# Kernel tuning notes

Measured on AMD Instinct MI355X. Metric: run time of the kernel, lower is better.

The kernel has to match this reference:

```python
import jax, jax.numpy as jnp
import numpy as np

NHEAD = 6
EPS = 1.1920929e-07  # torch RMSNorm default eps = finfo(float32).eps


def _rms(x, g):
    return x * jax.lax.rsqrt(jnp.mean(x * x, axis=-1, keepdims=True) + EPS) * g


def _mha(q, k, v):
    # q: [B, Sq, Hq, D]; k, v: [B, Sk, Hk, D] with Hk == Hq or Hk == 1 (broadcast)
    d = q.shape[-1]
    qh = q.transpose(0, 2, 1, 3)            # [B, Hq, Sq, D]
    kh = k.transpose(0, 2, 1, 3)            # [B, Hk, Sk, D]
    vh = v.transpose(0, 2, 1, 3)
    s = jnp.matmul(qh, kh.transpose(0, 1, 3, 2)) * (1.0 / np.sqrt(d).astype(np.float32))
    a = jax.nn.softmax(s, axis=-1)
    return jnp.matmul(a, vh).transpose(0, 2, 1, 3)  # [B, Sq, Hq, D]


def setup_inputs() -> dict:
    key = jax.random.key(0)
    B, R, G, E, L = 4, 1024, 8, 192, 4
    F = 2 * E  # dim_feedforward = emsize * 2
    ks = jax.random.split(key, 12)

    def w(k, shape):
        return jax.random.normal(k, shape, jnp.float32) * 0.02

    return {
        "hidden": jax.random.normal(ks[0], (B, R, G, E), jnp.float32),
        "Wq1": w(ks[1], (L, E, E)), "Wk1": w(ks[2], (L, E, E)),
        "Wv1": w(ks[3], (L, E, E)), "Wo1": w(ks[4], (L, E, E)),
        "Wq2": w(ks[5], (L, E, E)), "Wk2": w(ks[6], (L, E, E)),
        "Wv2": w(ks[7], (L, E, E)), "Wo2": w(ks[8], (L, E, E)),
        "W1": w(ks[9], (L, E, F)), "W2": w(ks[10], (L, F, E)),
        "g1": jnp.ones((L, E), jnp.float32),
        "g2": jnp.ones((L, E), jnp.float32),
        "g3": jnp.ones((L, E), jnp.float32),
        "single_eval_pos": 768,
    }


def reference(hidden, Wq1, Wk1, Wv1, Wo1, Wq2, Wk2, Wv2, Wo2, W1, W2, g1, g2, g3, single_eval_pos):
    B, R, G, E = hidden.shape
    H, D = NHEAD, E // NHEAD
    sep = int(single_eval_pos)
    L = Wq1.shape[0]
    x = hidden
    for i in range(L):
        # --- per-sample attention between feature groups: seqs of length G ---
        xf = x.reshape(B * R, G, E)
        q = (xf @ Wq1[i]).reshape(B * R, G, H, D)
        k = (xf @ Wk1[i]).reshape(B * R, G, H, D)
        v = (xf @ Wv1[i]).reshape(B * R, G, H, D)
        xf = xf + _mha(q, k, v).reshape(B * R, G, E) @ Wo1[i]
        # --- along-column attention over rows with train/test split ---
        xr = _rms(xf, g1[i]).reshape(B, R, G, E).transpose(0, 2, 1, 3).reshape(B * G, R, E)
        q = (xr @ Wq2[i]).reshape(B * G, R, H, D)
        k = (xr[:, :sep] @ Wk2[i]).reshape(B * G, sep, H, D)
        v = (xr[:, :sep] @ Wv2[i]).reshape(B * G, sep, H, D)
        train_out = _mha(q[:, :sep], k, v)
        # test rows attend to first head's keys/values only (broadcast over heads)
        test_out = _mha(q[:, sep:], k[:, :, :1], v[:, :, :1])
        attn = jnp.concatenate([train_out, test_out], axis=1).reshape(B * G, R, E) @ Wo2[i]
        xc = _rms(xr + attn, g2[i])
        # --- MLP (exact GELU) + final RMSNorm ---
        x = xc.reshape(B, G, R, E).transpose(0, 2, 1, 3)
        x = x + jax.nn.gelu(x @ W1[i], approximate=False) @ W2[i]
        x = _rms(x, g3[i])
    return x
```

## Files before the change

### kernel.cpp

```cpp
#include <hip/hip_runtime.h>
#include <hip/hip_bf16.h>
#include <math.h>

#define B_ 4
#define R_ 1024
#define G_ 8
#define E_ 192
#define H_ 6
#define D_ 32
#define L_ 4
#define F_ 384
#define M_ (B_*R_*G_)
static const size_t NBUF = (size_t)M_ * E_;
static const size_t WPL  = 8 * (size_t)E_ * E_ + 2 * (size_t)E_ * F_;

typedef __attribute__((ext_vector_type(8))) short bf16x8;
typedef __attribute__((ext_vector_type(8))) unsigned short u16x8;
typedef __attribute__((ext_vector_type(4))) float f32x4;

__device__ __forceinline__ float gelu_exact(float x) {
    return 0.5f * x * (1.0f + erff(x * 0.7071067811865475f));
}
__device__ __forceinline__ unsigned short f2bf(float f) {
    __hip_bfloat16 h = __float2bfloat16(f);
    return *(unsigned short*)&h;
}
__device__ __forceinline__ float bf2f(unsigned short h) {
    union { unsigned u; float f; } v; v.u = ((unsigned)h) << 16; return v.f;
}
__device__ __forceinline__ bf16x8 mk8(unsigned long long lo, unsigned long long hi) {
    union { unsigned long long q[2]; bf16x8 v; } u;
    u.q[0] = lo; u.q[1] = hi; return u.v;
}

__global__ __launch_bounds__(256)
void k_convw_all(const float* __restrict__ Wq1, const float* __restrict__ Wk1,
                 const float* __restrict__ Wv1, const float* __restrict__ Wo1,
                 const float* __restrict__ Wq2, const float* __restrict__ Wk2,
                 const float* __restrict__ Wv2, const float* __restrict__ Wo2,
                 const float* __restrict__ W1,  const float* __restrict__ W2,
                 unsigned short* __restrict__ Wt)
{
    const int t = blockIdx.x;
    const int layer = t / 432;
    const int r = t % 432;
    const float* src; unsigned short* dst; int K, N; float scale = 1.f; int tile;
    if (r < 288) {
        const int w = r / 36; tile = r % 36; K = E_; N = E_;
        const float* tab[8] = {Wq1, Wk1, Wv1, Wo1, Wq2, Wk2, Wv2, Wo2};
        src = tab[w] + (size_t)layer * E_ * E_;
        dst = Wt + (size_t)layer * WPL + (size_t)w * E_ * E_;
        if (w == 0) scale = 0.17677669529663687f;
        if (w == 4) scale = 0.17677669529663687f * 1.4426950408889634f;
    } else if (r < 360) {
        tile = r - 288; K = E_; N = F_;
        src = W1 + (size_t)layer * E_ * F_;
        dst = Wt + (size_t)layer * WPL + 8 * (size_t)E_ * E_;
    } else {
        tile = r - 360; K = F_; N = E_;
        src = W2 + (size_t)layer * E_ * F_;
        dst = Wt + (size_t)layer * WPL + 8 * (size_t)E_ * E_ + (size_t)E_ * F_;
    }
    const int ntx = N / 32;
    const int kb = (tile / ntx) * 32, nb = (tile % ntx) * 32;
    __shared__ float tl[32][33];
    const int tx = threadIdx.x & 31, ty = threadIdx.x >> 5;
    for (int i2 = 0; i2 < 32; i2 += 8)
        tl[ty + i2][tx] = src[(size_t)(kb + ty + i2) * N + nb + tx];
    __syncthreads();
    for (int i2 = 0; i2 < 32; i2 += 8)
        dst[(size_t)(nb + ty + i2) * K + kb + tx] = f2bf(tl[tx][ty + i2] * scale);
}

template<bool ABF16, int EPI>
__global__ __launch_bounds__(256)
void k_gemm_mfma(const void* __restrict__ Ap, const unsigned short* __restrict__ Wt,
                 void* __restrict__ Cp, int ldc, int K)
{
    __shared__ unsigned short As[64][40];
    __shared__ unsigned short Bs[192][40];
    const int m0 = blockIdx.x * 64;
    const int n0 = blockIdx.y * 192;
    const int tid = threadIdx.x;
    const int w = tid >> 6, lane = tid & 63, l15 = lane & 15, g = lane >> 4;
    const int arow = tid >> 2, akoff = (tid & 3) << 3;
    f32x4 acc[4][3];
#pragma unroll
    for (int mt = 0; mt < 4; ++mt)
#pragma unroll
        for (int nt = 0; nt < 3; ++nt)
#pragma unroll
            for (int r2 = 0; r2 < 4; ++r2) acc[mt][nt][r2] = 0.f;
    const int nK = K >> 5;

    float4 ax, ay; u16x8 av; u16x8 bv0, bv1, bv2;
    auto gload = [&](int k0) {
        if (ABF16) {
            av = *(const u16x8*)((const unsigned short*)Ap + (size_t)(m0 + arow) * K + k0 + akoff);
        } else {
            const float* ap = (const float*)Ap + (size_t)(m0 + arow) * K + k0 + akoff;
            ax = *(const float4*)ap; ay = *(const float4*)(ap + 4);
        }
        bv0 = *(const u16x8*)(Wt + (size_t)(n0 + arow      ) * K + k0 + akoff);
        bv1 = *(const u16x8*)(Wt + (size_t)(n0 + arow +  64) * K + k0 + akoff);
        bv2 = *(const u16x8*)(Wt + (size_t)(n0 + arow + 128) * K + k0 + akoff);
    };
    auto swrite = [&]() {
        u16x8 aw;
        if (ABF16) aw = av;
        else {
            aw[0] = f2bf(ax.x); aw[1] = f2bf(ax.y); aw[2] = f2bf(ax.z); aw[3] = f2bf(ax.w);
            aw[4] = f2bf(ay.x); aw[5] = f2bf(ay.y); aw[6] = f2bf(ay.z); aw[7] = f2bf(ay.w);
        }
        *(u16x8*)&As[arow][akoff] = aw;
        *(u16x8*)&Bs[arow][akoff] = bv0;
        *(u16x8*)&Bs[arow + 64][akoff] = bv1;
        *(u16x8*)&Bs[arow + 128][akoff] = bv2;
    };

    gload(0);
    for (int kc = 0; kc < nK; ++kc) {
        __syncthreads();
        swrite();
        __syncthreads();
        if (kc + 1 < nK) gload((kc + 1) << 5);
        bf16x8 af[4], bfr[3];
#pragma unroll
        for (int mt = 0; mt < 4; ++mt) af[mt] = *(const bf16x8*)&As[mt * 16 + l15][g * 8];
#pragma unroll
        for (int nt = 0; nt < 3; ++nt) bfr[nt] = *(const bf16x8*)&Bs[w * 48 + nt * 16 + l15][g * 8];
#pragma unroll
        for (int mt = 0; mt < 4; ++mt)
#pragma unroll
            for (int nt = 0; nt < 3; ++nt)
                acc[mt][nt] = __builtin_amdgcn_mfma_f32_16x16x32_bf16(af[mt], bfr[nt], acc[mt][nt], 0, 0, 0);
    }

#pragma unroll
    for (int mt = 0; mt < 4; ++mt)
#pragma unroll
        for (int r2 = 0; r2 < 4; ++r2) {
            const int m = m0 + mt * 16 + g * 4 + r2;
#pragma unroll
            for (int nt = 0; nt < 3; ++nt) {
                const int n = w * 48 + nt * 16 + l15;
                float v = acc[mt][nt][r2];
                if (EPI == 1) v = gelu_exact(v);
                ((unsigned short*)Cp)[(size_t)m * ldc + n0 + n] = f2bf(v);
            }
        }
}

template<bool RESBF16, int EPI>
__global__ __launch_bounds__(256)
void k_gemm_rms32(const unsigned short* __restrict__ Ap, const unsigned short* __restrict__ Wt,
                  const void* __restrict__ Resp, const float* __restrict__ gvec,
                  void* __restrict__ Cp, int K)
{
    __shared__ unsigned short As[32][40];
    __shared__ unsigned short Bs[192][40];
    __shared__ float ss_red[4][16];
    const int m0 = blockIdx.x * 32;
    const int tid = threadIdx.x;
    const int w = tid >> 6, lane = tid & 63, l15 = lane & 15, g = lane >> 4;
    const int mt = w & 1, nh = w >> 1;
    const int arow = tid >> 2, akoff = (tid & 3) << 3;
    f32x4 acc[6];
#pragma unroll
    for (int nt = 0; nt < 6; ++nt)
#pragma unroll
        for (int r2 = 0; r2 < 4; ++r2) acc[nt][r2] = 0.f;
    const int nK = K >> 5;

    u16x8 av, bv0, bv1, bv2;
    auto gload = [&](int k0) {
        if (tid < 128)
            av = *(const u16x8*)(Ap + (size_t)(m0 + arow) * K + k0 + akoff);
        bv0 = *(const u16x8*)(Wt + (size_t)(arow      ) * K + k0 + akoff);
        bv1 = *(const u16x8*)(Wt + (size_t)(arow +  64) * K + k0 + akoff);
        bv2 = *(const u16x8*)(Wt + (size_t)(arow + 128) * K + k0 + akoff);
    };
    auto swrite = [&]() {
        if (tid < 128) *(u16x8*)&As[arow][akoff] = av;
        *(u16x8*)&Bs[arow][akoff] = bv0;
        *(u16x8*)&Bs[arow + 64][akoff] = bv1;
        *(u16x8*)&Bs[arow + 128][akoff] = bv2;
    };

    gload(0);
    for (int kc = 0; kc < nK; ++kc) {
        __syncthreads();
        swrite();
        __syncthreads();
        if (kc + 1 < nK) gload((kc + 1) << 5);
        bf16x8 af = *(const bf16x8*)&As[mt * 16 + l15][g * 8];
        bf16x8 bfr[6];
#pragma unroll
        for (int nt = 0; nt < 6; ++nt) bfr[nt] = *(const bf16x8*)&Bs[nh * 96 + nt * 16 + l15][g * 8];
#pragma unroll
        for (int nt = 0; nt < 6; ++nt)
            acc[nt] = __builtin_amdgcn_mfma_f32_16x16x32_bf16(af, bfr[nt], acc[nt], 0, 0, 0);
    }

    float ssp[4] = {0.f, 0.f, 0.f, 0.f};
#pragma unroll
    for (int r2 = 0; r2 < 4; ++r2) {
        const int m = m0 + mt * 16 + g * 4 + r2;
#pragma unroll
        for (int nt = 0; nt < 6; ++nt) {
            const int n = nh * 96 + nt * 16 + l15;
            float rres = RESBF16 ? bf2f(((const unsigned short*)Resp)[(size_t)m * E_ + n])
                                 : ((const float*)Resp)[(size_t)m * E_ + n];
            float v = acc[nt][r2] + rres;
            acc[nt][r2] = v;
            ssp[r2] += v * v;
        }
    }
#pragma unroll
    for (int off = 1; off < 16; off <<= 1)
#pragma unroll
        for (int r2 = 0; r2 < 4; ++r2)
            ssp[r2] += __shfl_xor(ssp[r2], off);
    if (l15 == 0) {
#pragma unroll
        for (int r2 = 0; r2 < 4; ++r2)
            ss_red[w][g * 4 + r2] = ssp[r2];
    }
    __syncthreads();
#pragma unroll
    for (int r2 = 0; r2 < 4; ++r2) {
        const int lr = g * 4 + r2;
        const float ss = ss_red[mt][lr] + ss_red[2 + mt][lr];
        const float inv = rsqrtf(ss * (1.0f / 192.0f) + 1.1920929e-07f);
        const int m = m0 + mt * 16 + lr;
        size_t orow;
        if (EPI == 2) {
            const int b = m >> 13, rr = (m >> 3) & 1023, gg = m & 7;
            orow = (((size_t)b * G_ + gg) << 10) + rr;
        } else if (EPI == 3) {
            const int b = m >> 13, gg = (m >> 10) & 7, rr = m & 1023;
            orow = ((((size_t)b << 10) + rr) << 3) + gg;
        } else {
            orow = m;
        }
#pragma unroll
        for (int nt = 0; nt < 6; ++nt) {
            const int n = nh * 96 + nt * 16 + l15;
            const float v = acc[nt][r2] * inv * gvec[n];
            if (EPI == 4) ((float*)Cp)[orow * E_ + n] = v;
            else          ((unsigned short*)Cp)[orow * E_ + n] = f2bf(v);
        }
    }
}

__global__ __launch_bounds__(256)
void k_attn1(const unsigned short* __restrict__ QKV, unsigned short* __restrict__ T)
{
    const int wave = blockIdx.x * 4 + (threadIdx.x >> 6);
    const int lane = threadIdx.x & 63;
    const int seq = wave / H_;
    const int h = wave % H_;
    const int i = lane >> 3, j = lane & 7;
    const unsigned short* qp = QKV + ((size_t)(seq * G_ + i)) * 576 + h * D_;
    const unsigned short* kp = QKV + ((size_t)(seq * G_ + j)) * 576 + 192 + h * D_;
    float s = 0.f;
#pragma unroll
    for (int d8 = 0; d8 < 4; ++d8) {
        u16x8 qv = *(const u16x8*)(qp + d8 * 8);
        u16x8 kv = *(const u16x8*)(kp + d8 * 8);
#pragma unroll
        for (int e = 0; e < 8; ++e) s += bf2f(qv[e]) * bf2f(kv[e]);
    }
    float mx = s;
#pragma unroll
    for (int off = 1; off < 8; off <<= 1) mx = fmaxf(mx, __shfl_xor(mx, off));
    float p = __expf(s - mx);
    float sum = p;
#pragma unroll
    for (int off = 1; off < 8; off <<= 1) sum += __shfl_xor(sum, off);
    p /= sum;
    const int base = lane & ~7;
    float o0 = 0.f, o1 = 0.f, o2 = 0.f, o3 = 0.f;
#pragma unroll
    for (int jj = 0; jj < 8; ++jj) {
        float pj = __shfl(p, base + jj);
        ushort4 vv = *(const ushort4*)(QKV + ((size_t)(seq * G_ + jj)) * 576 + 384 + h * D_ + j * 4);
        o0 += pj * bf2f(vv.x); o1 += pj * bf2f(vv.y);
        o2 += pj * bf2f(vv.z); o3 += pj * bf2f(vv.w);
    }
    ushort4 ov; ov.x = f2bf(o0); ov.y = f2bf(o1); ov.z = f2bf(o2); ov.w = f2bf(o3);
    *(ushort4*)(T + ((size_t)(seq * G_ + i)) * E_ + h * D_ + j * 4) = ov;
}

__global__ __launch_bounds__(256)
void k_attn2(const unsigned short* __restrict__ QKV, unsigned short* __restrict__ T,
             const int* __restrict__ sep_ptr)
{
    __shared__ __align__(16) unsigned short K_lds[64][40];
    __shared__ __align__(16) unsigned short V_lds[2048];

    const int sep = *sep_ptr;
    const int bid = blockIdx.x;
    const int sh = ((bid >> 7) << 3) | (bid & 7);
    const int qtile = (bid >> 3) & 15;
    const int s = sh / H_, h = sh % H_;
    const int q0 = qtile * 64;

    const int tid = threadIdx.x;
    const int w = tid >> 6;
    const int lane = tid & 63;
    const int l15 = lane & 15;
    const int g = lane >> 4;

    const int qrow = q0 + w * 16 + l15;
    u16x8 qf = *(const u16x8*)(QKV + ((size_t)s * R_ + qrow) * 576 + h * D_ + g * 8);

    u16x8 onesu;
#pragma unroll
    for (int e = 0; e < 8; ++e) onesu[e] = 0x3F80;
    const bf16x8 onesf = (bf16x8)onesu;

    const bool lo = (q0 < sep);
    const bool hi = (q0 + 64 > sep);
    const int npass = (lo && hi) ? 2 : 1;
    const int nChunk = (sep + 63) >> 6;

    const int skey = tid >> 2;
    const int sg   = tid & 3;
    const int vst = ((sg >> 1) * 16 + (skey >> 2)) * 64 + (skey & 3) * 16 + (sg & 1) * 8;
    const unsigned vaddr = (unsigned)(size_t)&V_lds[0] + (unsigned)(g * 128 + l15 * 2);

    for (int pass = 0; pass < npass; ++pass) {
        const int hk = (pass == 0) ? (lo ? h : 0) : 0;
        const unsigned short* Kb = QKV + (size_t)s * R_ * 576 + 192 + hk * D_;
        const unsigned short* Vb = QKV + (size_t)s * R_ * 576 + 384 + hk * D_;

        float mrun = -1e30f;
        f32x4 o0 = {0.f, 0.f, 0.f, 0.f};
        f32x4 o1 = {0.f, 0.f, 0.f, 0.f};
        f32x4 o2 = {0.f, 0.f, 0.f, 0.f};

        u16x8 kv_k = *(const u16x8*)(Kb + (size_t)skey * 576 + sg * 8);
        u16x8 kv_v = *(const u16x8*)(Vb + (size_t)skey * 576 + sg * 8);

        for (int kc = 0; kc < nChunk; ++kc) {
            const int kbase = kc * 64;
            const bool full = (kbase + 64 <= sep);
            __syncthreads();
            *(u16x8*)&K_lds[skey][sg * 8] = kv_k;
            *(u16x8*)&V_lds[vst] = kv_v;
            __syncthreads();
            if (kc + 1 < nChunk) {
                kv_k = *(const u16x8*)(Kb + (size_t)(kbase + 64 + skey) * 576 + sg * 8);
                kv_v = *(const u16x8*)(Vb + (size_t)(kbase + 64 + skey) * 576 + sg * 8);
            }

            f32x4 sc[4];
            const f32x4 zf = {0.f, 0.f, 0.f, 0.f};
            __builtin_amdgcn_s_setprio(1);
#pragma unroll
            for (int t = 0; t < 4; ++t) {
                bf16x8 a = *(const bf16x8*)&K_lds[t * 16 + l15][g * 8];
                sc[t] = __builtin_amdgcn_mfma_f32_16x16x32_bf16(a, (bf16x8)qf, zf, 0, 0, 0);
            }
            __builtin_amdgcn_s_setprio(0);
            if (!full) {
#pragma unroll
                for (int t = 0; t < 4; ++t)
#pragma unroll
                    for (int r = 0; r < 4; ++r)
                        if (kbase + t * 16 + g * 4 + r >= sep) sc[t][r] = -1e30f;
            }
            float mx = fmaxf(fmaxf(sc[0][0], sc[0][1]), sc[0][2]);
            mx = fmaxf(fmaxf(sc[0][3], sc[1][0]), mx);
            mx = fmaxf(fmaxf(sc[1][1], sc[1][2]), mx);
            mx = fmaxf(fmaxf(sc[1][3], sc[2][0]), mx);
            mx = fmaxf(fmaxf(sc[2][1], sc[2][2]), mx);
            mx = fmaxf(fmaxf(sc[2][3], sc[3][0]), mx);
            mx = fmaxf(fmaxf(sc[3][1], sc[3][2]), mx);
            mx = fmaxf(mx, sc[3][3]);
            if (!__all((int)(mx <= mrun + 11.0f))) {
                mx = fmaxf(mx, __shfl_xor(mx, 16));
                mx = fmaxf(mx, __shfl_xor(mx, 32));
                const float mnew = fmaxf(mrun, mx);
                const float scl = exp2f(mrun - mnew);
#pragma unroll
                for (int r = 0; r < 4; ++r) { o0[r] *= scl; o1[r] *= scl; o2[r] *= scl; }
                mrun = mnew;
            }
            bf16x8 pb0, pb1;
            {
                u16x8 p0, p1;
#pragma unroll
                for (int r = 0; r < 4; ++r) {
                    p0[r]     = f2bf(exp2f(sc[0][r] - mrun));
                    p0[4 + r] = f2bf(exp2f(sc[1][r] - mrun));
                    p1[r]     = f2bf(exp2f(sc[2][r] - mrun));
                    p1[4 + r] = f2bf(exp2f(sc[3][r] - mrun));
                }
                pb0 = (bf16x8)p0; pb1 = (bf16x8)p1;
            }
            unsigned long long t0, t1, t2, t3, t4, t5, t6, t7;
            asm volatile(
                "ds_read_b64_tr_b16 %0, %8 offset:0\n\t"
                "ds_read_b64_tr_b16 %1, %8 offset:512\n\t"
                "ds_read_b64_tr_b16 %2, %8 offset:1024\n\t"
                "ds_read_b64_tr_b16 %3, %8 offset:1536\n\t"
                "ds_read_b64_tr_b16 %4, %8 offset:2048\n\t"
                "ds_read_b64_tr_b16 %5, %8 offset:2560\n\t"
                "ds_read_b64_tr_b16 %6, %8 offset:3072\n\t"
                "ds_read_b64_tr_b16 %7, %8 offset:3584\n\t"
                "s_waitcnt lgkmcnt(0)"
                : "=&v"(t0), "=&v"(t1), "=&v"(t2), "=&v"(t3),
                  "=&v"(t4), "=&v"(t5), "=&v"(t6), "=&v"(t7)
                : "v"(vaddr)
                : "memory");
            __builtin_amdgcn_sched_barrier(0);
            __builtin_amdgcn_s_setprio(1);
            o0 = __builtin_amdgcn_mfma_f32_16x16x32_bf16(mk8(t0, t1), pb0, o0, 0, 0, 0);
            o1 = __builtin_amdgcn_mfma_f32_16x16x32_bf16(mk8(t4, t5), pb0, o1, 0, 0, 0);
            o2 = __builtin_amdgcn_mfma_f32_16x16x32_bf16(onesf,       pb0, o2, 0, 0, 0);
            o0 = __builtin_amdgcn_mfma_f32_16x16x32_bf16(mk8(t2, t3), pb1, o0, 0, 0, 0);
            o1 = __builtin_amdgcn_mfma_f32_16x16x32_bf16(mk8(t6, t7), pb1, o1, 0, 0, 0);
            o2 = __builtin_amdgcn_mfma_f32_16x16x32_bf16(onesf,       pb1, o2, 0, 0, 0);
            __builtin_amdgcn_s_setprio(0);
        }

        const bool valid = (npass == 1) || (pass == 0 ? (qrow < sep) : (qrow >= sep));
        if (valid) {
            const float inv = 1.f / o2[0];
            unsigned short* tp = T + ((size_t)s * R_ + qrow) * E_ + h * D_;
            ushort4 v0, v1;
            v0.x = f2bf(o0[0] * inv); v0.y = f2bf(o0[1] * inv);
            v0.z = f2bf(o0[2] * inv); v0.w = f2bf(o0[3] * inv);
            v1.x = f2bf(o1[0] * inv); v1.y = f2bf(o1[1] * inv);
            v1.z = f2bf(o1[2] * inv); v1.w = f2bf(o1[3] * inv);
            *(ushort4*)(tp + g * 4)      = v0;
            *(ushort4*)(tp + 16 + g * 4) = v1;
        }
    }
}

extern "C" void kernel_launch(void* const* d_in, const int* in_sizes, int n_in,
                              void* d_out, int out_size, void* d_ws, size_t ws_size,
                              hipStream_t stream) {
    const float* hidden = (const float*)d_in[0];
    const float* Wq1 = (const float*)d_in[1];
    const float* Wk1 = (const float*)d_in[2];
    const float* Wv1 = (const float*)d_in[3];
    const float* Wo1 = (const float*)d_in[4];
    const float* Wq2 = (const float*)d_in[5];
    const float* Wk2 = (const float*)d_in[6];
    const float* Wv2 = (const float*)d_in[7];
    const float* Wo2 = (const float*)d_in[8];
    const float* W1  = (const float*)d_in[9];
    const float* W2  = (const float*)d_in[10];
    const float* g1  = (const float*)d_in[11];
    const float* g2  = (const float*)d_in[12];
    const float* g3  = (const float*)d_in[13];
    const int*   sep = (const int*)d_in[14];

    float* Xout = (float*)d_out;
    unsigned short* ws = (unsigned short*)d_ws;
    unsigned short* QKVb = ws;
    unsigned short* Tb   = QKVb + (size_t)M_ * 576;
    unsigned short* Ynb  = Tb + NBUF;
    unsigned short* Xcb  = Ynb + NBUF;
    unsigned short* Xb   = Xcb + NBUF;
    unsigned short* Wt   = Xb + NBUF;
    unsigned short* H1b  = QKVb;

    const dim3 blk(256);
    const dim3 gQKV(M_ / 64, 3);
    const dim3 gW1(M_ / 64, 2);
    const dim3 g32(M_ / 32);
    const dim3 gA1((4096 * H_) / 4);
    const dim3 gA2(32 * H_ * 16);

    k_convw_all<<<dim3(432 * L_), blk, 0, stream>>>(Wq1, Wk1, Wv1, Wo1, Wq2, Wk2, Wv2, Wo2, W1, W2, Wt);

    for (int i = 0; i < L_; ++i) {
        unsigned short* wl = Wt + (size_t)i * WPL;
        const unsigned short* wqkv1 = wl;
        const unsigned short* wo1   = wl + 3 * (size_t)E_ * E_;
        const unsigned short* wqkv2 = wl + 4 * (size_t)E_ * E_;
        const unsigned short* wo2   = wl + 7 * (size_t)E_ * E_;
        const unsigned short* w1    = wl + 8 * (size_t)E_ * E_;
        const unsigned short* w2    = wl + 8 * (size_t)E_ * E_ + (size_t)E_ * F_;
        const float* g1i = g1 + (size_t)i * E_;
        const float* g2i = g2 + (size_t)i * E_;
        const float* g3i = g3 + (size_t)i * E_;

        if (i == 0)
            k_gemm_mfma<false, 0><<<gQKV, blk, 0, stream>>>(hidden, wqkv1, QKVb, 576, E_);
        else
            k_gemm_mfma<true, 0><<<gQKV, blk, 0, stream>>>(Xb, wqkv1, QKVb, 576, E_);
        k_attn1<<<gA1, blk, 0, stream>>>(QKVb, Tb);
        if (i == 0)
            k_gemm_rms32<false, 2><<<g32, blk, 0, stream>>>(Tb, wo1, hidden, g1i, Ynb, E_);
        else
            k_gemm_rms32<true, 2><<<g32, blk, 0, stream>>>(Tb, wo1, Xb, g1i, Ynb, E_);
        k_gemm_mfma<true, 0><<<gQKV, blk, 0, stream>>>(Ynb, wqkv2, QKVb, 576, E_);
        k_attn2<<<gA2, blk, 0, stream>>>(QKVb, Tb, sep);
        k_gemm_rms32<true, 3><<<g32, blk, 0, stream>>>(Tb, wo2, Ynb, g2i, Xcb, E_);
        k_gemm_mfma<true, 1><<<gW1, blk, 0, stream>>>(Xcb, w1, H1b, F_, E_);
        if (i == L_ - 1)
            k_gemm_rms32<true, 4><<<g32, blk, 0, stream>>>(H1b, w2, Xcb, g3i, Xout, F_);
        else
            k_gemm_rms32<true, 5><<<g32, blk, 0, stream>>>(H1b, w2, Xcb, g3i, Xb, F_);
    }
}
```

Measured before the change: 683.1 us.

## Process two query tiles per wave in column attention to reuse K/V LDS loads

Each attention block now covers 128 query rows instead of 64, with every wave handling two 16-row query fragments against the same K and V fragments read from LDS. The aim is to halve global K/V loads and LDS staging per query row and to amortise the sync and LDS reads across more MFMA work. In exchange, register pressure rises from the doubled accumulators and the grid is halved, which lowers parallelism and occupancy. The NBUF change is cosmetic.

```diff
diff --git a/kernel.cpp b/kernel.cpp
--- a/kernel.cpp
+++ b/kernel.cpp
@@ -11,7 +11,7 @@
 #define L_ 4
 #define F_ 384
 #define M_ (B_*R_*G_)
-static const size_t NBUF = (size_t)M_ * E_;
+static const size_t NBUF = (size_t)M_ * 192;
 static const size_t WPL  = 8 * (size_t)E_ * E_ + 2 * (size_t)E_ * F_;
 
 typedef __attribute__((ext_vector_type(8))) short bf16x8;
@@ -301,10 +301,10 @@
 
     const int sep = *sep_ptr;
     const int bid = blockIdx.x;
-    const int sh = ((bid >> 7) << 3) | (bid & 7);
-    const int qtile = (bid >> 3) & 15;
+    const int sh = ((bid >> 6) << 3) | (bid & 7);
+    const int qtile = (bid >> 3) & 7;
     const int s = sh / H_, h = sh % H_;
-    const int q0 = qtile * 64;
+    const int q0 = qtile * 128;
 
     const int tid = threadIdx.x;
     const int w = tid >> 6;
@@ -312,8 +312,9 @@
     const int l15 = lane & 15;
     const int g = lane >> 4;
 
-    const int qrow = q0 + w * 16 + l15;
-    u16x8 qf = *(const u16x8*)(QKV + ((size_t)s * R_ + qrow) * 576 + h * D_ + g * 8);
+    const int qrow0 = q0 + w * 32 + l15;
+    u16x8 qf0 = *(const u16x8*)(QKV + ((size_t)s * R_ + qrow0) * 576 + h * D_ + g * 8);
+    u16x8 qf1 = *(const u16x8*)(QKV + ((size_t)s * R_ + qrow0 + 16) * 576 + h * D_ + g * 8);
 
     u16x8 onesu;
 #pragma unroll
@@ -321,7 +322,7 @@
     const bf16x8 onesf = (bf16x8)onesu;
 
     const bool lo = (q0 < sep);
-    const bool hi = (q0 + 64 > sep);
+    const bool hi = (q0 + 128 > sep);
     const int npass = (lo && hi) ? 2 : 1;
     const int nChunk = (sep + 63) >> 6;
 
@@ -335,10 +336,9 @@
         const unsigned short* Kb = QKV + (size_t)s * R_ * 576 + 192 + hk * D_;
         const unsigned short* Vb = QKV + (size_t)s * R_ * 576 + 384 + hk * D_;
 
-        float mrun = -1e30f;
-        f32x4 o0 = {0.f, 0.f, 0.f, 0.f};
-        f32x4 o1 = {0.f, 0.f, 0.f, 0.f};
-        f32x4 o2 = {0.f, 0.f, 0.f, 0.f};
+        float m0r = -1e30f, m1r = -1e30f;
+        f32x4 o0a = {0.f,0.f,0.f,0.f}, o0b = {0.f,0.f,0.f,0.f}, o0c = {0.f,0.f,0.f,0.f};
+        f32x4 o1a = {0.f,0.f,0.f,0.f}, o1b = {0.f,0.f,0.f,0.f}, o1c = {0.f,0.f,0.f,0.f};
 
         u16x8 kv_k = *(const u16x8*)(Kb + (size_t)skey * 576 + sg * 8);
         u16x8 kv_v = *(const u16x8*)(Vb + (size_t)skey * 576 + sg * 8);
@@ -355,51 +355,10 @@
                 kv_v = *(const u16x8*)(Vb + (size_t)(kbase + 64 + skey) * 576 + sg * 8);
             }
 
-            f32x4 sc[4];
-            const f32x4 zf = {0.f, 0.f, 0.f, 0.f};
-            __builtin_amdgcn_s_setprio(1);
-#pragma unroll
-            for (int t = 0; t < 4; ++t) {
-                bf16x8 a = *(const bf16x8*)&K_lds[t * 16 + l15][g * 8];
-                sc[t] = __builtin_amdgcn_mfma_f32_16x16x32_bf16(a, (bf16x8)qf, zf, 0, 0, 0);
-            }
-            __builtin_amdgcn_s_setprio(0);
-            if (!full) {
-#pragma unroll
-                for (int t = 0; t < 4; ++t)
-#pragma unroll
-                    for (int r = 0; r < 4; ++r)
-                        if (kbase + t * 16 + g * 4 + r >= sep) sc[t][r] = -1e30f;
-            }
-            float mx = fmaxf(fmaxf(sc[0][0], sc[0][1]), sc[0][2]);
-            mx = fmaxf(fmaxf(sc[0][3], sc[1][0]), mx);
-            mx = fmaxf(fmaxf(sc[1][1], sc[1][2]), mx);
-            mx = fmaxf(fmaxf(sc[1][3], sc[2][0]), mx);
-            mx = fmaxf(fmaxf(sc[2][1], sc[2][2]), mx);
-            mx = fmaxf(fmaxf(sc[2][3], sc[3][0]), mx);
-            mx = fmaxf(fmaxf(sc[3][1], sc[3][2]), mx);
-            mx = fmaxf(mx, sc[3][3]);
-            if (!__all((int)(mx <= mrun + 11.0f))) {
-                mx = fmaxf(mx, __shfl_xor(mx, 16));
-                mx = fmaxf(mx, __shfl_xor(mx, 32));
-                const float mnew = fmaxf(mrun, mx);
-                const float scl = exp2f(mrun - mnew);
-#pragma unroll
-                for (int r = 0; r < 4; ++r) { o0[r] *= scl; o1[r] *= scl; o2[r] *= scl; }
-                mrun = mnew;
-            }
-            bf16x8 pb0, pb1;
-            {
-                u16x8 p0, p1;
-#pragma unroll
-                for (int r = 0; r < 4; ++r) {
-                    p0[r]     = f2bf(exp2f(sc[0][r] - mrun));
-                    p0[4 + r] = f2bf(exp2f(sc[1][r] - mrun));
-                    p1[r]     = f2bf(exp2f(sc[2][r] - mrun));
-                    p1[4 + r] = f2bf(exp2f(sc[3][r] - mrun));
-                }
-                pb0 = (bf16x8)p0; pb1 = (bf16x8)p1;
-            }
+            bf16x8 kfr0 = *(const bf16x8*)&K_lds[l15][g * 8];
+            bf16x8 kfr1 = *(const bf16x8*)&K_lds[16 + l15][g * 8];
+            bf16x8 kfr2 = *(const bf16x8*)&K_lds[32 + l15][g * 8];
+            bf16x8 kfr3 = *(const bf16x8*)&K_lds[48 + l15][g * 8];
             unsigned long long t0, t1, t2, t3, t4, t5, t6, t7;
             asm volatile(
                 "ds_read_b64_tr_b16 %0, %8 offset:0\n\t"
@@ -416,28 +375,82 @@
                 : "v"(vaddr)
                 : "memory");
             __builtin_amdgcn_sched_barrier(0);
-            __builtin_amdgcn_s_setprio(1);
-            o0 = __builtin_amdgcn_mfma_f32_16x16x32_bf16(mk8(t0, t1), pb0, o0, 0, 0, 0);
-            o1 = __builtin_amdgcn_mfma_f32_16x16x32_bf16(mk8(t4, t5), pb0, o1, 0, 0, 0);
-            o2 = __builtin_amdgcn_mfma_f32_16x16x32_bf16(onesf,       pb0, o2, 0, 0, 0);
-            o0 = __builtin_amdgcn_mfma_f32_16x16x32_bf16(mk8(t2, t3), pb1, o0, 0, 0, 0);
-            o1 = __builtin_amdgcn_mfma_f32_16x16x32_bf16(mk8(t6, t7), pb1, o1, 0, 0, 0);
-            o2 = __builtin_amdgcn_mfma_f32_16x16x32_bf16(onesf,       pb1, o2, 0, 0, 0);
-            __builtin_amdgcn_s_setprio(0);
-        }
-
-        const bool valid = (npass == 1) || (pass == 0 ? (qrow < sep) : (qrow >= sep));
-        if (valid) {
-            const float inv = 1.f / o2[0];
-            unsigned short* tp = T + ((size_t)s * R_ + qrow) * E_ + h * D_;
-            ushort4 v0, v1;
-            v0.x = f2bf(o0[0] * inv); v0.y = f2bf(o0[1] * inv);
-            v0.z = f2bf(o0[2] * inv); v0.w = f2bf(o0[3] * inv);
-            v1.x = f2bf(o1[0] * inv); v1.y = f2bf(o1[1] * inv);
-            v1.z = f2bf(o1[2] * inv); v1.w = f2bf(o1[3] * inv);
-            *(ushort4*)(tp + g * 4)      = v0;
-            *(ushort4*)(tp + 16 + g * 4) = v1;
-        }
+
+            auto process = [&](const u16x8& qf, float& mrun,
+                               f32x4& oa, f32x4& ob, f32x4& oc) {
+                f32x4 sc[4];
+                const f32x4 zf = {0.f, 0.f, 0.f, 0.f};
+                __builtin_amdgcn_s_setprio(1);
+                sc[0] = __builtin_amdgcn_mfma_f32_16x16x32_bf16(kfr0, (bf16x8)qf, zf, 0, 0, 0);
+                sc[1] = __builtin_amdgcn_mfma_f32_16x16x32_bf16(kfr1, (bf16x8)qf, zf, 0, 0, 0);
+                sc[2] = __builtin_amdgcn_mfma_f32_16x16x32_bf16(kfr2, (bf16x8)qf, zf, 0, 0, 0);
+                sc[3] = __builtin_amdgcn_mfma_f32_16x16x32_bf16(kfr3, (bf16x8)qf, zf, 0, 0, 0);
+                __builtin_amdgcn_s_setprio(0);
+                if (!full) {
+#pragma unroll
+                    for (int t = 0; t < 4; ++t)
+#pragma unroll
+                        for (int r = 0; r < 4; ++r)
+                            if (kbase + t * 16 + g * 4 + r >= sep) sc[t][r] = -1e30f;
+                }
+                float mx = fmaxf(fmaxf(sc[0][0], sc[0][1]), sc[0][2]);
+                mx = fmaxf(fmaxf(sc[0][3], sc[1][0]), mx);
+                mx = fmaxf(fmaxf(sc[1][1], sc[1][2]), mx);
+                mx = fmaxf(fmaxf(sc[1][3], sc[2][0]), mx);
+                mx = fmaxf(fmaxf(sc[2][1], sc[2][2]), mx);
+                mx = fmaxf(fmaxf(sc[2][3], sc[3][0]), mx);
+                mx = fmaxf(fmaxf(sc[3][1], sc[3][2]), mx);
+                mx = fmaxf(mx, sc[3][3]);
+                if (!__all((int)(mx <= mrun + 11.0f))) {
+                    mx = fmaxf(mx, __shfl_xor(mx, 16));
+                    mx = fmaxf(mx, __shfl_xor(mx, 32));
+                    const float mnew = fmaxf(mrun, mx);
+                    const float scl = exp2f(mrun - mnew);
+#pragma unroll
+                    for (int r = 0; r < 4; ++r) { oa[r] *= scl; ob[r] *= scl; oc[r] *= scl; }
+                    mrun = mnew;
+                }
+                bf16x8 pb0, pb1;
+                {
+                    u16x8 p0, p1;
+#pragma unroll
+                    for (int r = 0; r < 4; ++r) {
+                        p0[r]     = f2bf(exp2f(sc[0][r] - mrun));
+                        p0[4 + r] = f2bf(exp2f(sc[1][r] - mrun));
+                        p1[r]     = f2bf(exp2f(sc[2][r] - mrun));
+                        p1[4 + r] = f2bf(exp2f(sc[3][r] - mrun));
+                    }
+                    pb0 = (bf16x8)p0; pb1 = (bf16x8)p1;
+                }
+                __builtin_amdgcn_s_setprio(1);
+                oa = __builtin_amdgcn_mfma_f32_16x16x32_bf16(mk8(t0, t1), pb0, oa, 0, 0, 0);
+                ob = __builtin_amdgcn_mfma_f32_16x16x32_bf16(mk8(t4, t5), pb0, ob, 0, 0, 0);
+                oc = __builtin_amdgcn_mfma_f32_16x16x32_bf16(onesf,       pb0, oc, 0, 0, 0);
+                oa = __builtin_amdgcn_mfma_f32_16x16x32_bf16(mk8(t2, t3), pb1, oa, 0, 0, 0);
+                ob = __builtin_amdgcn_mfma_f32_16x16x32_bf16(mk8(t6, t7), pb1, ob, 0, 0, 0);
+                oc = __builtin_amdgcn_mfma_f32_16x16x32_bf16(onesf,       pb1, oc, 0, 0, 0);
+                __builtin_amdgcn_s_setprio(0);
+            };
+            process(qf0, m0r, o0a, o0b, o0c);
+            process(qf1, m1r, o1a, o1b, o1c);
+        }
+
+        auto epi = [&](int qrow, const f32x4& oa, const f32x4& ob, const f32x4& oc) {
+            const bool valid = (npass == 1) || (pass == 0 ? (qrow < sep) : (qrow >= sep));
+            if (valid) {
+                const float inv = 1.f / oc[0];
+                unsigned short* tp = T + ((size_t)s * R_ + qrow) * E_ + h * D_;
+                ushort4 v0, v1;
+                v0.x = f2bf(oa[0] * inv); v0.y = f2bf(oa[1] * inv);
+                v0.z = f2bf(oa[2] * inv); v0.w = f2bf(oa[3] * inv);
+                v1.x = f2bf(ob[0] * inv); v1.y = f2bf(ob[1] * inv);
+                v1.z = f2bf(ob[2] * inv); v1.w = f2bf(ob[3] * inv);
+                *(ushort4*)(tp + g * 4)      = v0;
+                *(ushort4*)(tp + 16 + g * 4) = v1;
+            }
+        };
+        epi(qrow0,      o0a, o0b, o0c);
+        epi(qrow0 + 16, o1a, o1b, o1c);
     }
 }
 
@@ -475,7 +488,7 @@
     const dim3 gW1(M_ / 64, 2);
     const dim3 g32(M_ / 32);
     const dim3 gA1((4096 * H_) / 4);
-    const dim3 gA2(32 * H_ * 16);
+    const dim3 gA2(32 * H_ * 8);
 
     k_convw_all<<<dim3(432 * L_), blk, 0, stream>>>(Wq1, Wk1, Wv1, Wo1, Wq2, Wk2, Wv2, Wo2, W1, W2, Wt);
 
```

Result: slower. 725.2 us (+6.2%).

## Fuse feature-group attention block (QKV GEMM, attention, Wo GEMM, RMSNorm) into one kernel

Applied to the files above, without the earlier changes.

Replaces the three-kernel sequence for the per-sample feature attention (QKV projection GEMM, k_attn1, Wo GEMM with residual and RMSNorm) with a single kernel per 32-row tile. Each tile of 32 rows covers exactly 4 sequences of 8 groups, so QKV stays in LDS, attention runs from LDS, and the output projection plus norm happen in place. This removes the global-memory round trips of the QKV and attention-output buffers and two launches per layer. In exchange it uses large LDS (about 60 KB), which lowers occupancy, and it has many syncthreads-bound serial phases with less MFMA parallelism per block.

```diff
diff --git a/kernel.cpp b/kernel.cpp
--- a/kernel.cpp
+++ b/kernel.cpp
@@ -253,43 +253,187 @@
     }
 }
 
+template<bool AF32>
 __global__ __launch_bounds__(256)
-void k_attn1(const unsigned short* __restrict__ QKV, unsigned short* __restrict__ T)
+void k_featblock(const void* __restrict__ Xin, const unsigned short* __restrict__ Wqkv,
+                 const unsigned short* __restrict__ Wo, const float* __restrict__ gvec,
+                 unsigned short* __restrict__ Ynb)
 {
-    const int wave = blockIdx.x * 4 + (threadIdx.x >> 6);
-    const int lane = threadIdx.x & 63;
-    const int seq = wave / H_;
-    const int h = wave % H_;
-    const int i = lane >> 3, j = lane & 7;
-    const unsigned short* qp = QKV + ((size_t)(seq * G_ + i)) * 576 + h * D_;
-    const unsigned short* kp = QKV + ((size_t)(seq * G_ + j)) * 576 + 192 + h * D_;
-    float s = 0.f;
-#pragma unroll
-    for (int d8 = 0; d8 < 4; ++d8) {
-        u16x8 qv = *(const u16x8*)(qp + d8 * 8);
-        u16x8 kv = *(const u16x8*)(kp + d8 * 8);
-#pragma unroll
-        for (int e = 0; e < 8; ++e) s += bf2f(qv[e]) * bf2f(kv[e]);
-    }
-    float mx = s;
-#pragma unroll
-    for (int off = 1; off < 8; off <<= 1) mx = fmaxf(mx, __shfl_xor(mx, off));
-    float p = __expf(s - mx);
-    float sum = p;
-#pragma unroll
-    for (int off = 1; off < 8; off <<= 1) sum += __shfl_xor(sum, off);
-    p /= sum;
-    const int base = lane & ~7;
-    float o0 = 0.f, o1 = 0.f, o2 = 0.f, o3 = 0.f;
-#pragma unroll
-    for (int jj = 0; jj < 8; ++jj) {
-        float pj = __shfl(p, base + jj);
-        ushort4 vv = *(const ushort4*)(QKV + ((size_t)(seq * G_ + jj)) * 576 + 384 + h * D_ + j * 4);
-        o0 += pj * bf2f(vv.x); o1 += pj * bf2f(vv.y);
-        o2 += pj * bf2f(vv.z); o3 += pj * bf2f(vv.w);
-    }
-    ushort4 ov; ov.x = f2bf(o0); ov.y = f2bf(o1); ov.z = f2bf(o2); ov.w = f2bf(o3);
-    *(ushort4*)(T + ((size_t)(seq * G_ + i)) * E_ + h * D_ + j * 4) = ov;
+    __shared__ __align__(16) unsigned char raw[576 * 40 * 2];
+    __shared__ __align__(16) unsigned short As[32][40];
+    __shared__ __align__(16) unsigned short Tl[32][200];
+    __shared__ float ss_red[4][32];
+
+    unsigned short (*Bq)[40]    = (unsigned short (*)[40])raw;
+    unsigned short (*QKVl)[584] = (unsigned short (*)[584])raw;
+    unsigned short (*Bo)[40]    = (unsigned short (*)[40])raw;
+
+    const int m0 = blockIdx.x * 32;
+    const int tid = threadIdx.x;
+    const int w = tid >> 6, lane = tid & 63, l15 = lane & 15, g = lane >> 4;
+    const int arow = (tid & 127) >> 2, akoff = (tid & 3) << 3;
+
+    f32x4 acc[2][9];
+#pragma unroll
+    for (int mt = 0; mt < 2; ++mt)
+#pragma unroll
+        for (int nt = 0; nt < 9; ++nt)
+#pragma unroll
+            for (int r2 = 0; r2 < 4; ++r2) acc[mt][nt][r2] = 0.f;
+
+    for (int kc = 0; kc < 6; ++kc) {
+        const int k0 = kc << 5;
+        __syncthreads();
+        if (tid < 128) {
+            u16x8 aw;
+            if (AF32) {
+                const float* ap = (const float*)Xin + (size_t)(m0 + arow) * E_ + k0 + akoff;
+                float4 x = *(const float4*)ap, y = *(const float4*)(ap + 4);
+                aw[0] = f2bf(x.x); aw[1] = f2bf(x.y); aw[2] = f2bf(x.z); aw[3] = f2bf(x.w);
+                aw[4] = f2bf(y.x); aw[5] = f2bf(y.y); aw[6] = f2bf(y.z); aw[7] = f2bf(y.w);
+            } else {
+                aw = *(const u16x8*)((const unsigned short*)Xin + (size_t)(m0 + arow) * E_ + k0 + akoff);
+            }
+            *(u16x8*)&As[arow][akoff] = aw;
+        }
+#pragma unroll
+        for (int j = 0; j < 9; ++j) {
+            const int v = tid + 256 * j;
+            const int br = v >> 2, bk = (v & 3) << 3;
+            *(u16x8*)&Bq[br][bk] = *(const u16x8*)(Wqkv + (size_t)br * E_ + k0 + bk);
+        }
+        __syncthreads();
+        bf16x8 af0 = *(const bf16x8*)&As[l15][g * 8];
+        bf16x8 af1 = *(const bf16x8*)&As[16 + l15][g * 8];
+#pragma unroll
+        for (int nt = 0; nt < 9; ++nt) {
+            bf16x8 bf = *(const bf16x8*)&Bq[w * 144 + nt * 16 + l15][g * 8];
+            acc[0][nt] = __builtin_amdgcn_mfma_f32_16x16x32_bf16(af0, bf, acc[0][nt], 0, 0, 0);
+            acc[1][nt] = __builtin_amdgcn_mfma_f32_16x16x32_bf16(af1, bf, acc[1][nt], 0, 0, 0);
+        }
+    }
+    __syncthreads();
+#pragma unroll
+    for (int mt = 0; mt < 2; ++mt)
+#pragma unroll
+        for (int r2 = 0; r2 < 4; ++r2)
+#pragma unroll
+            for (int nt = 0; nt < 9; ++nt)
+                QKVl[mt * 16 + g * 4 + r2][w * 144 + nt * 16 + l15] = f2bf(acc[mt][nt][r2]);
+    __syncthreads();
+
+    {
+        const int i = lane >> 3, j = lane & 7;
+        const int r0 = w * 8;
+#pragma unroll
+        for (int h = 0; h < 6; ++h) {
+            float s = 0.f;
+#pragma unroll
+            for (int d8 = 0; d8 < 4; ++d8) {
+                u16x8 qv = *(const u16x8*)&QKVl[r0 + i][h * 32 + d8 * 8];
+                u16x8 kv = *(const u16x8*)&QKVl[r0 + j][192 + h * 32 + d8 * 8];
+#pragma unroll
+                for (int e = 0; e < 8; ++e) s += bf2f(qv[e]) * bf2f(kv[e]);
+            }
+            float mx = s;
+#pragma unroll
+            for (int off = 1; off < 8; off <<= 1) mx = fmaxf(mx, __shfl_xor(mx, off));
+            float p = __expf(s - mx);
+            float sum = p;
+#pragma unroll
+            for (int off = 1; off < 8; off <<= 1) sum += __shfl_xor(sum, off);
+            p /= sum;
+            const int base = lane & ~7;
+            float o0 = 0.f, o1 = 0.f, o2 = 0.f, o3 = 0.f;
+#pragma unroll
+            for (int jj = 0; jj < 8; ++jj) {
+                float pj = __shfl(p, base + jj);
+                ushort4 vv = *(const ushort4*)&QKVl[r0 + jj][384 + h * 32 + j * 4];
+                o0 += pj * bf2f(vv.x); o1 += pj * bf2f(vv.y);
+                o2 += pj * bf2f(vv.z); o3 += pj * bf2f(vv.w);
+            }
+            ushort4 ov; ov.x = f2bf(o0); ov.y = f2bf(o1); ov.z = f2bf(o2); ov.w = f2bf(o3);
+            *(ushort4*)&Tl[r0 + i][h * 32 + j * 4] = ov;
+        }
+    }
+    __syncthreads();
+
+    f32x4 acc2[2][3];
+#pragma unroll
+    for (int mt = 0; mt < 2; ++mt)
+#pragma unroll
+        for (int nt = 0; nt < 3; ++nt)
+#pragma unroll
+            for (int r2 = 0; r2 < 4; ++r2) acc2[mt][nt][r2] = 0.f;
+
+    for (int kc = 0; kc < 6; ++kc) {
+        const int k0 = kc << 5;
+        __syncthreads();
+#pragma unroll
+        for (int j = 0; j < 3; ++j) {
+            const int v = tid + 256 * j;
+            const int br = v >> 2, bk = (v & 3) << 3;
+            *(u16x8*)&Bo[br][bk] = *(const u16x8*)(Wo + (size_t)br * E_ + k0 + bk);
+        }
+        __syncthreads();
+        bf16x8 af0 = *(const bf16x8*)&Tl[l15][k0 + g * 8];
+        bf16x8 af1 = *(const bf16x8*)&Tl[16 + l15][k0 + g * 8];
+#pragma unroll
+        for (int nt = 0; nt < 3; ++nt) {
+            bf16x8 bf = *(const bf16x8*)&Bo[w * 48 + nt * 16 + l15][g * 8];
+            acc2[0][nt] = __builtin_amdgcn_mfma_f32_16x16x32_bf16(af0, bf, acc2[0][nt], 0, 0, 0);
+            acc2[1][nt] = __builtin_amdgcn_mfma_f32_16x16x32_bf16(af1, bf, acc2[1][nt], 0, 0, 0);
+        }
+    }
+    __syncthreads();
+
+    float ssp[2][4] = {};
+#pragma unroll
+    for (int mt = 0; mt < 2; ++mt)
+#pragma unroll
+        for (int r2 = 0; r2 < 4; ++r2) {
+            const int m = m0 + mt * 16 + g * 4 + r2;
+#pragma unroll
+            for (int nt = 0; nt < 3; ++nt) {
+                const int n = w * 48 + nt * 16 + l15;
+                float rres = AF32 ? ((const float*)Xin)[(size_t)m * E_ + n]
+                                  : bf2f(((const unsigned short*)Xin)[(size_t)m * E_ + n]);
+                float v = acc2[mt][nt][r2] + rres;
+                acc2[mt][nt][r2] = v;
+                ssp[mt][r2] += v * v;
+            }
+        }
+#pragma unroll
+    for (int off = 1; off < 16; off <<= 1)
+#pragma unroll
+        for (int mt = 0; mt < 2; ++mt)
+#pragma unroll
+            for (int r2 = 0; r2 < 4; ++r2)
+                ssp[mt][r2] += __shfl_xor(ssp[mt][r2], off);
+    if (l15 == 0) {
+#pragma unroll
+        for (int mt = 0; mt < 2; ++mt)
+#pragma unroll
+            for (int r2 = 0; r2 < 4; ++r2)
+                ss_red[w][mt * 16 + g * 4 + r2] = ssp[mt][r2];
+    }
+    __syncthreads();
+#pragma unroll
+    for (int mt = 0; mt < 2; ++mt)
+#pragma unroll
+        for (int r2 = 0; r2 < 4; ++r2) {
+            const int row = mt * 16 + g * 4 + r2;
+            const float ss = ss_red[0][row] + ss_red[1][row] + ss_red[2][row] + ss_red[3][row];
+            const float inv = rsqrtf(ss * (1.0f / 192.0f) + 1.1920929e-07f);
+            const int m = m0 + row;
+            const int b = m >> 13, rr = (m >> 3) & 1023, gg = m & 7;
+            const size_t orow = (((size_t)(b * G_ + gg)) << 10) + rr;
+#pragma unroll
+            for (int nt = 0; nt < 3; ++nt) {
+                const int n = w * 48 + nt * 16 + l15;
+                Ynb[orow * E_ + n] = f2bf(acc2[mt][nt][r2] * inv * gvec[n]);
+            }
+        }
 }
 
 __global__ __launch_bounds__(256)
@@ -474,7 +618,6 @@
     const dim3 gQKV(M_ / 64, 3);
     const dim3 gW1(M_ / 64, 2);
     const dim3 g32(M_ / 32);
-    const dim3 gA1((4096 * H_) / 4);
     const dim3 gA2(32 * H_ * 16);
 
     k_convw_all<<<dim3(432 * L_), blk, 0, stream>>>(Wq1, Wk1, Wv1, Wo1, Wq2, Wk2, Wv2, Wo2, W1, W2, Wt);
@@ -492,14 +635,9 @@
         const float* g3i = g3 + (size_t)i * E_;
 
         if (i == 0)
-            k_gemm_mfma<false, 0><<<gQKV, blk, 0, stream>>>(hidden, wqkv1, QKVb, 576, E_);
+            k_featblock<true><<<g32, blk, 0, stream>>>(hidden, wqkv1, wo1, g1i, Ynb);
         else
-            k_gemm_mfma<true, 0><<<gQKV, blk, 0, stream>>>(Xb, wqkv1, QKVb, 576, E_);
-        k_attn1<<<gA1, blk, 0, stream>>>(QKVb, Tb);
-        if (i == 0)
-            k_gemm_rms32<false, 2><<<g32, blk, 0, stream>>>(Tb, wo1, hidden, g1i, Ynb, E_);
-        else
-            k_gemm_rms32<true, 2><<<g32, blk, 0, stream>>>(Tb, wo1, Xb, g1i, Ynb, E_);
+            k_featblock<false><<<g32, blk, 0, stream>>>(Xb, wqkv1, wo1, g1i, Ynb);
         k_gemm_mfma<true, 0><<<gQKV, blk, 0, stream>>>(Ynb, wqkv2, QKVb, 576, E_);
         k_attn2<<<gA2, blk, 0, stream>>>(QKVb, Tb, sep);
         k_gemm_rms32<true, 3><<<g32, blk, 0, stream>>>(Tb, wo2, Ynb, g2i, Xcb, E_);
```

Result: faster. 641.6 us (-6.1%).
